# Performance work log

Hardware: AMD Instinct MI355X
Metric: run time of the kernel (lower is better)

Reference implementation:

```python
import jax, jax.numpy as jnp
import numpy as np

NUM_NODES = 100_000
NUM_EDGES = 1_200_000
NUM_REL = 3
EMBED_DIM = 64
HIDDEN_DIM = 64
NUM_CLS = 2
NUM_GRAPHS = 512


def setup_inputs() -> dict:
    key = jax.random.key(0)
    ks = jax.random.split(key, 12)
    s = 1.0 / np.sqrt(EMBED_DIM)
    inp = {
        # forward args
        "x": jnp.zeros((NUM_NODES,), dtype=jnp.int64),  # vocab size 1 -> all zeros
        "edge_index": jax.random.randint(ks[0], (2, NUM_EDGES), 0, NUM_NODES, dtype=jnp.int64),
        "edge_type": jax.random.randint(ks[1], (NUM_EDGES,), 0, NUM_REL, dtype=jnp.int64),
        "batch": jnp.sort(jax.random.randint(ks[2], (NUM_NODES,), 0, NUM_GRAPHS, dtype=jnp.int64)),
        # parameters
        "embed_w": jax.random.normal(ks[3], (1, EMBED_DIM), jnp.float32),
        "W1": jax.random.normal(ks[4], (NUM_REL, EMBED_DIM, HIDDEN_DIM), jnp.float32) * s,
        "root1": jax.random.normal(ks[5], (EMBED_DIM, HIDDEN_DIM), jnp.float32) * s,
        "b1": jnp.zeros((HIDDEN_DIM,), jnp.float32),
        "W2": jax.random.normal(ks[6], (NUM_REL, HIDDEN_DIM, HIDDEN_DIM), jnp.float32) * s,
        "root2": jax.random.normal(ks[7], (HIDDEN_DIM, HIDDEN_DIM), jnp.float32) * s,
        "b2": jnp.zeros((HIDDEN_DIM,), jnp.float32),
        "lin_w": jax.random.normal(ks[8], (HIDDEN_DIM, NUM_CLS), jnp.float32) * s,
        "lin_b": jnp.zeros((NUM_CLS,), jnp.float32),
    }
    return inp


def rgcn_conv(h, W, root, b, src, dst, edge_type):
    """PyG RGCNConv with mean aggregation per relation + root weight + bias."""
    n = h.shape[0]
    out = h @ root + b  # root/self contribution, [N, H]
    for r in range(NUM_REL):
        m = (edge_type == r).astype(h.dtype)  # [E]
        tr = h @ W[r]                          # [N, H] small GEMM
        msg = tr[src] * m[:, None]             # gather [E, H]
        ssum = jax.ops.segment_sum(msg, dst, num_segments=n)  # scatter-add [N, H]
        cnt = jax.ops.segment_sum(m, dst, num_segments=n)     # per-relation in-degree
        out = out + ssum / jnp.clip(cnt, 1.0)[:, None]        # mean aggregation
    return out


def reference(x, edge_index, edge_type, batch, embed_w, W1, root1, b1, W2, root2, b2, lin_w, lin_b):
    src, dst = edge_index[0], edge_index[1]
    h = embed_w[x]                                       # [N, D] embedding lookup
    h = jax.nn.relu(rgcn_conv(h, W1, root1, b1, src, dst, edge_type))
    h = jax.nn.relu(rgcn_conv(h, W2, root2, b2, src, dst, edge_type))
    # global mean pool over graphs
    gsum = jax.ops.segment_sum(h, batch, num_segments=NUM_GRAPHS)            # [G, H]
    gcnt = jax.ops.segment_sum(jnp.ones_like(h[:, 0]), batch, num_segments=NUM_GRAPHS)
    g_emb = gsum / jnp.clip(gcnt, 1.0)[:, None]
    return g_emb @ lin_w + lin_b                          # [G, num_cls]
```

## Files before the change

### kernel.cpp

```cpp
#include <hip/hip_runtime.h>

#define NODES   100000
#define EDGES   1200000
#define NREL    3
#define DIM     64
#define NGRAPH  512

#define BSH     7
#define NB      782
#define NBK2    782
#define BUCKCAP 2048
#define NCH     448
#define CHUNK   2680
#define POISON  0xAAAAAAAAu

#define OFF_PSUM  0
#define OFF_PCNT  4096
#define OFF_DONE  6144
#define OFF_ZEND  6400
#define OFF_CUR   6400
#define OFF_MBN   9600
#define OFF_REC   409984
#define OFF_BASE  6816128
#define OFF_T2    6818176

__global__ __launch_bounds__(512) void k_scat_tab(
        const int* __restrict__ ei, const int* __restrict__ et,
        const float* __restrict__ embed_w, const float* __restrict__ W1,
        const float* __restrict__ root1, const float* __restrict__ b1,
        const float* __restrict__ W2, const float* __restrict__ root2,
        const float* __restrict__ b2,
        unsigned int* __restrict__ cursor, unsigned int* __restrict__ rec,
        unsigned char* __restrict__ mbn,
        float* __restrict__ base, float* __restrict__ T2,
        char* __restrict__ ws) {
    const int tid = threadIdx.x;
    const int bid = blockIdx.x;
    if (bid < 32) {
        {
            uint4* z = (uint4*)ws;
            const int gt = bid * 512 + tid;
            if (gt < OFF_ZEND / 16) z[gt] = make_uint4(0, 0, 0, 0);
        }
        __shared__ float h0[DIM];
        __shared__ float u[DIM];
        __shared__ float t[NREL][DIM];
        __shared__ float h1s[8][DIM];
        __shared__ float red[4][DIM];
        const bool act = tid < 256;
        const int j = tid & 63, w = (tid >> 6) & 3;
        if (act && tid < DIM) h0[tid] = embed_w[tid];
        __syncthreads();
        if (act) {
            const float* M = (w == 0) ? root1 : (W1 + (size_t)(w - 1) * DIM * DIM);
            float s = 0.f;
            for (int k = 0; k < DIM; ++k) s += h0[k] * M[k * DIM + j];
            if (w == 0) u[j] = s + b1[j];
            else        t[w - 1][j] = s;
        }
        __syncthreads();
        if (act) {
            for (int p = w; p < 8; p += 4) {
                float v = u[j];
                if (p & 1) v += t[0][j];
                if (p & 2) v += t[1][j];
                if (p & 4) v += t[2][j];
                h1s[p][j] = fmaxf(v, 0.f);
            }
        }
        __syncthreads();
        const int row = bid;
        const int p = (row < 8) ? row : ((row - 8) & 7);
        if (act) {
            const float* M = (row < 8) ? root2
                                       : (W2 + (size_t)((row - 8) >> 3) * DIM * DIM);
            float s = 0.f;
            for (int k = w * 16; k < w * 16 + 16; ++k) s += h1s[p][k] * M[k * DIM + j];
            red[w][j] = s;
        }
        __syncthreads();
        if (act && w == 0) {
            const float v = red[0][j] + red[1][j] + red[2][j] + red[3][j];
            if (row < 8) base[p * DIM + j] = v + b2[j];
            else         T2[(row - 8) * DIM + j] = v;
        }
        return;
    }
    __shared__ unsigned int   srec[CHUNK];
    __shared__ unsigned short sbkt[CHUNK];
    __shared__ int hist[NB];
    __shared__ int cur[NB];
    for (int b = tid; b < NB; b += 512) hist[b] = 0;
    __syncthreads();
    const int e0 = (bid - 32) * CHUNK;
    const int* src = ei;
    const int* dst = ei + EDGES;
    for (int i = tid; i < CHUNK / 4; i += 512) {
        const int e = e0 + i * 4;
        if (e < EDGES) {
            const int4 s4 = *(const int4*)(src + e);
            const int4 d4 = *(const int4*)(dst + e);
            const int4 r4 = *(const int4*)(et + e);
            const int j = i * 4;
            srec[j + 0] = ((unsigned)(d4.x & 127) << 19) | ((unsigned)r4.x << 17) | (unsigned)s4.x;
            srec[j + 1] = ((unsigned)(d4.y & 127) << 19) | ((unsigned)r4.y << 17) | (unsigned)s4.y;
            srec[j + 2] = ((unsigned)(d4.z & 127) << 19) | ((unsigned)r4.z << 17) | (unsigned)s4.z;
            srec[j + 3] = ((unsigned)(d4.w & 127) << 19) | ((unsigned)r4.w << 17) | (unsigned)s4.w;
            sbkt[j + 0] = (unsigned short)(d4.x >> BSH);
            sbkt[j + 1] = (unsigned short)(d4.y >> BSH);
            sbkt[j + 2] = (unsigned short)(d4.z >> BSH);
            sbkt[j + 3] = (unsigned short)(d4.w >> BSH);
            atomicAdd(&hist[d4.x >> BSH], 1); atomicAdd(&hist[d4.y >> BSH], 1);
            atomicAdd(&hist[d4.z >> BSH], 1); atomicAdd(&hist[d4.w >> BSH], 1);
            mbn[d4.x * 4 + r4.x] = 1; mbn[d4.y * 4 + r4.y] = 1;
            mbn[d4.z * 4 + r4.z] = 1; mbn[d4.w * 4 + r4.w] = 1;
        }
    }
    __syncthreads();
    for (int b = tid; b < NB; b += 512) {
        const int h = hist[b];
        unsigned off = 0;
        if (h) off = atomicAdd(&cursor[b], (unsigned)h) - POISON;
        cur[b] = b * BUCKCAP + (int)off;
    }
    __syncthreads();
    int nl = EDGES - e0;
    if (nl > CHUNK) nl = CHUNK;
    for (int i = tid; i < nl; i += 512) {
        const int b = sbkt[i];
        const int p = atomicAdd(&cur[b], 1);
        if (p < (b + 1) * BUCKCAP) rec[p] = srec[i];
    }
}

__global__ __launch_bounds__(512) void k_node(
        const unsigned int* __restrict__ rec, const unsigned int* __restrict__ cursor,
        const unsigned char* __restrict__ mbn, const int* __restrict__ batch,
        const float* __restrict__ base, const float* __restrict__ T2,
        const float* __restrict__ lin_w, const float* __restrict__ lin_b,
        float* __restrict__ psum, int* __restrict__ pcnt,
        int* __restrict__ done, float* __restrict__ out) {
    __shared__ unsigned int h[1536];
    __shared__ float bs[8 * DIM];
    __shared__ float ts[24 * DIM];
    __shared__ int lastflag;
    const int tid = threadIdx.x;
    const unsigned* mbn32 = (const unsigned*)mbn;
    h[tid] = 0; h[tid + 512] = 0; h[tid + 1024] = 0;
    bs[tid] = base[tid];
    ts[tid] = T2[tid]; ts[tid + 512] = T2[tid + 512]; ts[tid + 1024] = T2[tid + 1024];
    __syncthreads();
    const int b = blockIdx.x;
    const int s = b * BUCKCAP;
    const unsigned un = cursor[b] - POISON;
    const int n = (un > BUCKCAP) ? BUCKCAP : (int)un;
    for (int i = tid; i < n; i += 512) {
        const unsigned r32 = rec[s + i];
        const unsigned x = mbn32[r32 & 0x1FFFF];
        const int p = (x & 1) | ((x >> 7) & 2) | ((x >> 14) & 4);
        const int idx = (int)((r32 >> 19) & 127) * 24 + (int)((r32 >> 17) & 3) * 8 + p;
        atomicAdd(&h[idx >> 1], 1u << ((idx & 1) * 16));
    }
    __syncthreads();
    const int lane = tid & 63;
    const int w = tid >> 6;
    const int v0 = (b << BSH) + w * 16;
    float dummy = 0.f;
    if (v0 < NODES) {
        const float lw0 = lin_w[lane * 2 + 0];
        const float lw1 = lin_w[lane * 2 + 1];
        int pidx = v0 + (lane & 15);
        if (pidx >= NODES) pidx = NODES - 1;
        const int bv = batch[pidx];
        const int mv = (int)mbn32[pidx];
        float acc = 0.f;
        int curg = -1, runlen = 0;
        for (int i = 0; i < 16; ++i) {
            const int v = v0 + i;
            if (v >= NODES) break;
            const int mx = __shfl(mv, i);
            const int pm = (mx & 1) | ((mx >> 7) & 2) | ((mx >> 14) & 4);
            float sacc = bs[pm * DIM + lane];
            const unsigned* hv = &h[(v & 127) * 12];
            #pragma unroll
            for (int r = 0; r < NREL; ++r) {
                const unsigned x0 = hv[r * 4 + 0], x1 = hv[r * 4 + 1];
                const unsigned x2 = hv[r * 4 + 2], x3 = hv[r * 4 + 3];
                const int cr = (int)((x0 & 0xFFFF) + (x0 >> 16) + (x1 & 0xFFFF) + (x1 >> 16)
                                   + (x2 & 0xFFFF) + (x2 >> 16) + (x3 & 0xFFFF) + (x3 >> 16));
                if (cr > 0) {
                    float msg = 0.f;
                    const float* tr = &ts[r * 8 * DIM + lane];
                    if (x0) msg += (float)(x0 & 0xFFFF) * tr[0 * DIM]
                                 + (float)(x0 >> 16)    * tr[1 * DIM];
                    if (x1) msg += (float)(x1 & 0xFFFF) * tr[2 * DIM]
                                 + (float)(x1 >> 16)    * tr[3 * DIM];
                    if (x2) msg += (float)(x2 & 0xFFFF) * tr[4 * DIM]
                                 + (float)(x2 >> 16)    * tr[5 * DIM];
                    if (x3) msg += (float)(x3 & 0xFFFF) * tr[6 * DIM]
                                 + (float)(x3 >> 16)    * tr[7 * DIM];
                    sacc += msg / (float)cr;
                }
            }
            sacc = fmaxf(sacc, 0.f);
            const int g = __shfl(bv, i);
            if (g != curg) {
                if (curg >= 0) {
                    float p0 = acc * lw0, p1 = acc * lw1;
                    #pragma unroll
                    for (int off = 32; off; off >>= 1) {
                        p0 += __shfl_down(p0, off);
                        p1 += __shfl_down(p1, off);
                    }
                    if (lane == 0) {
                        dummy += atomicAdd(&psum[curg * 2 + 0], p0);
                        dummy += atomicAdd(&psum[curg * 2 + 1], p1);
                        dummy += (float)atomicAdd(&pcnt[curg], runlen);
                    }
                }
                curg = g; acc = 0.f; runlen = 0;
            }
            acc += sacc; runlen++;
        }
        if (curg >= 0) {
            float p0 = acc * lw0, p1 = acc * lw1;
            #pragma unroll
            for (int off = 32; off; off >>= 1) {
                p0 += __shfl_down(p0, off);
                p1 += __shfl_down(p1, off);
            }
            if (lane == 0) {
                dummy += atomicAdd(&psum[curg * 2 + 0], p0);
                dummy += atomicAdd(&psum[curg * 2 + 1], p1);
                dummy += (float)atomicAdd(&pcnt[curg], runlen);
            }
        }
    }
    asm volatile("" :: "v"(dummy));
    __syncthreads();
    if (tid == 0) lastflag = (atomicAdd(done, 1) == NBK2 - 1) ? 1 : 0;
    __syncthreads();
    if (lastflag && tid < NGRAPH) {
        const float q0 = atomicAdd(&psum[tid * 2 + 0], 0.0f);
        const float q1 = atomicAdd(&psum[tid * 2 + 1], 0.0f);
        const int   c  = atomicAdd(&pcnt[tid], 0);
        const float inv = 1.0f / fmaxf((float)c, 1.0f);
        out[tid * 2 + 0] = q0 * inv + lin_b[0];
        out[tid * 2 + 1] = q1 * inv + lin_b[1];
    }
}

extern "C" void kernel_launch(void* const* d_in, const int* in_sizes, int n_in,
                              void* d_out, int out_size, void* d_ws, size_t ws_size,
                              hipStream_t stream) {
    const int*   ei      = (const int*)d_in[1];
    const int*   et      = (const int*)d_in[2];
    const int*   batch   = (const int*)d_in[3];
    const float* embed_w = (const float*)d_in[4];
    const float* W1      = (const float*)d_in[5];
    const float* root1   = (const float*)d_in[6];
    const float* b1      = (const float*)d_in[7];
    const float* W2      = (const float*)d_in[8];
    const float* root2   = (const float*)d_in[9];
    const float* b2      = (const float*)d_in[10];
    const float* lin_w   = (const float*)d_in[11];
    const float* lin_b   = (const float*)d_in[12];
    float* out = (float*)d_out;

    char* ws = (char*)d_ws;
    float*         psum = (float*)(ws + OFF_PSUM);
    int*           pcnt = (int*)(ws + OFF_PCNT);
    int*           done = (int*)(ws + OFF_DONE);
    unsigned int*  cur  = (unsigned int*)(ws + OFF_CUR);
    unsigned char* mbn  = (unsigned char*)(ws + OFF_MBN);
    unsigned int*  rec  = (unsigned int*)(ws + OFF_REC);
    float*         base = (float*)(ws + OFF_BASE);
    float*         T2   = (float*)(ws + OFF_T2);

    k_scat_tab<<<32 + NCH, 512, 0, stream>>>(ei, et, embed_w, W1, root1, b1, W2,
                                             root2, b2, cur, rec, mbn, base, T2,
                                             (char*)d_ws);
    k_node    <<<NBK2,     512, 0, stream>>>(rec, cur, mbn, batch, base, T2, lin_w,
                                             lin_b, psum, pcnt, done, out);
}
```

Measured before the change: 140.3 us.

## Split mask pass into its own kernel and bucket precomputed 16-bit histogram indices

Moves the mbn relation-mask writes into a separate first kernel that runs alongside the weight-table blocks. A new scatter kernel then looks up the source node's mask and computes the final histogram index before bucketing. Records shrink from 32-bit packed edges to 16-bit indices, and the node kernel drops its per-edge random mask gather. In exchange, the destination and edge-type arrays are read twice and there is one more kernel launch.

```diff
diff --git a/kernel.cpp b/kernel.cpp
--- a/kernel.cpp
+++ b/kernel.cpp
@@ -21,16 +21,15 @@
 #define OFF_CUR   6400
 #define OFF_MBN   9600
 #define OFF_REC   409984
-#define OFF_BASE  6816128
-#define OFF_T2    6818176
-
-__global__ __launch_bounds__(512) void k_scat_tab(
+#define OFF_BASE  3612032
+#define OFF_T2    3614080
+
+__global__ __launch_bounds__(512) void k_tab_mask(
         const int* __restrict__ ei, const int* __restrict__ et,
         const float* __restrict__ embed_w, const float* __restrict__ W1,
         const float* __restrict__ root1, const float* __restrict__ b1,
         const float* __restrict__ W2, const float* __restrict__ root2,
         const float* __restrict__ b2,
-        unsigned int* __restrict__ cursor, unsigned int* __restrict__ rec,
         unsigned char* __restrict__ mbn,
         float* __restrict__ base, float* __restrict__ T2,
         char* __restrict__ ws) {
@@ -86,13 +85,36 @@
         }
         return;
     }
-    __shared__ unsigned int   srec[CHUNK];
+    const int e0 = (bid - 32) * CHUNK;
+    const int* dst = ei + EDGES;
+    for (int i = tid; i < CHUNK / 4; i += 512) {
+        const int e = e0 + i * 4;
+        if (e < EDGES) {
+            const int4 d4 = *(const int4*)(dst + e);
+            const int4 r4 = *(const int4*)(et + e);
+            mbn[d4.x * 4 + r4.x] = 1;
+            mbn[d4.y * 4 + r4.y] = 1;
+            mbn[d4.z * 4 + r4.z] = 1;
+            mbn[d4.w * 4 + r4.w] = 1;
+        }
+    }
+}
+
+__global__ __launch_bounds__(512) void k_scat(
+        const int* __restrict__ ei, const int* __restrict__ et,
+        const unsigned char* __restrict__ mbn,
+        unsigned int* __restrict__ cursor, unsigned short* __restrict__ rec,
+        char* __restrict__ ws_unused) {
+    __shared__ unsigned short sidx[CHUNK];
     __shared__ unsigned short sbkt[CHUNK];
     __shared__ int hist[NB];
     __shared__ int cur[NB];
+    const int tid = threadIdx.x;
+    const int bid = blockIdx.x;
+    const unsigned* mbn32 = (const unsigned*)mbn;
     for (int b = tid; b < NB; b += 512) hist[b] = 0;
     __syncthreads();
-    const int e0 = (bid - 32) * CHUNK;
+    const int e0 = bid * CHUNK;
     const int* src = ei;
     const int* dst = ei + EDGES;
     for (int i = tid; i < CHUNK / 4; i += 512) {
@@ -101,19 +123,25 @@
             const int4 s4 = *(const int4*)(src + e);
             const int4 d4 = *(const int4*)(dst + e);
             const int4 r4 = *(const int4*)(et + e);
+            const unsigned xa = mbn32[s4.x];
+            const unsigned xb = mbn32[s4.y];
+            const unsigned xc = mbn32[s4.z];
+            const unsigned xd = mbn32[s4.w];
+            const int pa = (xa & 1) | ((xa >> 7) & 2) | ((xa >> 14) & 4);
+            const int pb = (xb & 1) | ((xb >> 7) & 2) | ((xb >> 14) & 4);
+            const int pc = (xc & 1) | ((xc >> 7) & 2) | ((xc >> 14) & 4);
+            const int pd = (xd & 1) | ((xd >> 7) & 2) | ((xd >> 14) & 4);
             const int j = i * 4;
-            srec[j + 0] = ((unsigned)(d4.x & 127) << 19) | ((unsigned)r4.x << 17) | (unsigned)s4.x;
-            srec[j + 1] = ((unsigned)(d4.y & 127) << 19) | ((unsigned)r4.y << 17) | (unsigned)s4.y;
-            srec[j + 2] = ((unsigned)(d4.z & 127) << 19) | ((unsigned)r4.z << 17) | (unsigned)s4.z;
-            srec[j + 3] = ((unsigned)(d4.w & 127) << 19) | ((unsigned)r4.w << 17) | (unsigned)s4.w;
+            sidx[j + 0] = (unsigned short)((d4.x & 127) * 24 + r4.x * 8 + pa);
+            sidx[j + 1] = (unsigned short)((d4.y & 127) * 24 + r4.y * 8 + pb);
+            sidx[j + 2] = (unsigned short)((d4.z & 127) * 24 + r4.z * 8 + pc);
+            sidx[j + 3] = (unsigned short)((d4.w & 127) * 24 + r4.w * 8 + pd);
             sbkt[j + 0] = (unsigned short)(d4.x >> BSH);
             sbkt[j + 1] = (unsigned short)(d4.y >> BSH);
             sbkt[j + 2] = (unsigned short)(d4.z >> BSH);
             sbkt[j + 3] = (unsigned short)(d4.w >> BSH);
             atomicAdd(&hist[d4.x >> BSH], 1); atomicAdd(&hist[d4.y >> BSH], 1);
             atomicAdd(&hist[d4.z >> BSH], 1); atomicAdd(&hist[d4.w >> BSH], 1);
-            mbn[d4.x * 4 + r4.x] = 1; mbn[d4.y * 4 + r4.y] = 1;
-            mbn[d4.z * 4 + r4.z] = 1; mbn[d4.w * 4 + r4.w] = 1;
         }
     }
     __syncthreads();
@@ -129,12 +157,12 @@
     for (int i = tid; i < nl; i += 512) {
         const int b = sbkt[i];
         const int p = atomicAdd(&cur[b], 1);
-        if (p < (b + 1) * BUCKCAP) rec[p] = srec[i];
+        if (p < (b + 1) * BUCKCAP) rec[p] = sidx[i];
     }
 }
 
 __global__ __launch_bounds__(512) void k_node(
-        const unsigned int* __restrict__ rec, const unsigned int* __restrict__ cursor,
+        const unsigned short* __restrict__ rec, const unsigned int* __restrict__ cursor,
         const unsigned char* __restrict__ mbn, const int* __restrict__ batch,
         const float* __restrict__ base, const float* __restrict__ T2,
         const float* __restrict__ lin_w, const float* __restrict__ lin_b,
@@ -155,10 +183,7 @@
     const unsigned un = cursor[b] - POISON;
     const int n = (un > BUCKCAP) ? BUCKCAP : (int)un;
     for (int i = tid; i < n; i += 512) {
-        const unsigned r32 = rec[s + i];
-        const unsigned x = mbn32[r32 & 0x1FFFF];
-        const int p = (x & 1) | ((x >> 7) & 2) | ((x >> 14) & 4);
-        const int idx = (int)((r32 >> 19) & 127) * 24 + (int)((r32 >> 17) & 3) * 8 + p;
+        const int idx = rec[s + i];
         atomicAdd(&h[idx >> 1], 1u << ((idx & 1) * 16));
     }
     __syncthreads();
@@ -268,18 +293,18 @@
     float* out = (float*)d_out;
 
     char* ws = (char*)d_ws;
-    float*         psum = (float*)(ws + OFF_PSUM);
-    int*           pcnt = (int*)(ws + OFF_PCNT);
-    int*           done = (int*)(ws + OFF_DONE);
-    unsigned int*  cur  = (unsigned int*)(ws + OFF_CUR);
-    unsigned char* mbn  = (unsigned char*)(ws + OFF_MBN);
-    unsigned int*  rec  = (unsigned int*)(ws + OFF_REC);
-    float*         base = (float*)(ws + OFF_BASE);
-    float*         T2   = (float*)(ws + OFF_T2);
-
-    k_scat_tab<<<32 + NCH, 512, 0, stream>>>(ei, et, embed_w, W1, root1, b1, W2,
-                                             root2, b2, cur, rec, mbn, base, T2,
-                                             (char*)d_ws);
+    float*          psum = (float*)(ws + OFF_PSUM);
+    int*            pcnt = (int*)(ws + OFF_PCNT);
+    int*            done = (int*)(ws + OFF_DONE);
+    unsigned int*   cur  = (unsigned int*)(ws + OFF_CUR);
+    unsigned char*  mbn  = (unsigned char*)(ws + OFF_MBN);
+    unsigned short* rec  = (unsigned short*)(ws + OFF_REC);
+    float*          base = (float*)(ws + OFF_BASE);
+    float*          T2   = (float*)(ws + OFF_T2);
+
+    k_tab_mask<<<32 + NCH, 512, 0, stream>>>(ei, et, embed_w, W1, root1, b1, W2,
+                                             root2, b2, mbn, base, T2, (char*)d_ws);
+    k_scat    <<<NCH,      512, 0, stream>>>(ei, et, mbn, cur, rec, (char*)d_ws);
     k_node    <<<NBK2,     512, 0, stream>>>(rec, cur, mbn, batch, base, T2, lin_w,
                                              lin_b, psum, pcnt, done, out);
 }
```

New measurement: 142.8 us. About the same (+1.8%).
